# Optimization experiments

Measured on AMD Instinct MI355X. Metric: run time of the kernel, lower is better.

Reference implementation:

```python
import jax, jax.numpy as jnp
import numpy as np


def setup_inputs() -> dict:
    key = jax.random.key(0)
    k1, k2 = jax.random.split(key)
    b, n, d = 8, 8192, 512
    x = jax.random.normal(k1, (b, n, d), dtype=jnp.float32)
    # t holds 2n-2 Toeplitz coefficients per channel; forward only uses the first n rows.
    t = jax.random.normal(k2, (2 * n - 2, d), dtype=jnp.float32)
    return {"x": x, "t": t}


def reference(x, t):
    """Per-channel causal cumulative weighted sum (the math of the naive quadruple loop):
        o[i, u, j] = sum_{v=0}^{u} t[v, j] * x[i, v, j]
    x: (b, n, d), t: (2n-2, d) -> o: (b, n, d)
    """
    n = x.shape[1]
    # broadcast t over batch, fuse elementwise product, then inclusive cumsum along seq
    return jnp.cumsum(x * t[None, :n, :], axis=1)
```

## Files before the change

### kernel.cpp

```cpp
#include <hip/hip_runtime.h>


typedef float f4 __attribute__((ext_vector_type(4)));

#define D  512
#define DV (D / 4)
#define C  128
#define RS 4

__global__ __launch_bounds__(DV * RS) void k_chunksum(
    const float* __restrict__ x, const float* __restrict__ t,
    float* __restrict__ S, int b, int n, int L) {
  const int c  = blockIdx.x / b;
  const int i  = blockIdx.x % b;
  const int jv = threadIdx.x & (DV - 1);
  const int h  = threadIdx.x >> 7;
  const int rows = L / RS;
  const size_t row0 = (size_t)c * L + (size_t)h * rows;
  const f4* xp = (const f4*)x + ((size_t)i * n + row0) * DV + jv;
  const f4* tp = (const f4*)t + row0 * DV + jv;
  f4 acc = {0.f, 0.f, 0.f, 0.f};
#pragma unroll 8
  for (int v = 0; v < rows; ++v) {
    acc += xp[(size_t)v * DV] * tp[(size_t)v * DV];
  }
  __shared__ f4 red[RS][DV];
  red[h][jv] = acc;
  __syncthreads();
  if (h == 0) {
    f4 s = red[0][jv] + red[1][jv] + red[2][jv] + red[3][jv];
    ((f4*)S)[((size_t)c * b + i) * DV + jv] = s;
  }
}

__global__ __launch_bounds__(DV) void k_out(
    const float* __restrict__ x, const float* __restrict__ t,
    const float* __restrict__ S, float* __restrict__ o, int b, int n, int L) {
  const int c  = blockIdx.x / b;
  const int i  = blockIdx.x % b;
  const int jv = threadIdx.x;

  f4 acc = {0.f, 0.f, 0.f, 0.f};
  const f4* Sp = (const f4*)S + (size_t)i * DV + jv;
  const size_t cstride = (size_t)b * DV;
#pragma unroll 8
  for (int cp = 0; cp < c; ++cp) {
    acc += Sp[(size_t)cp * cstride];
  }

  const size_t row0  = (size_t)c * L;
  const size_t xbase = ((size_t)i * n + row0) * DV + jv;
  const f4* xp = (const f4*)x + xbase;
  const f4* tp = (const f4*)t + row0 * DV + jv;
  f4*       op = (f4*)o + xbase;
#pragma unroll 4
  for (int v = 0; v < L; ++v) {
    acc += xp[(size_t)v * DV] * tp[(size_t)v * DV];
    op[(size_t)v * DV] = acc;
  }
}

__global__ __launch_bounds__(256) void k_naive(
    const float* __restrict__ x, const float* __restrict__ t,
    float* __restrict__ o, int b, int n) {
  const int tid = blockIdx.x * 256 + threadIdx.x;
  if (tid >= b * DV) return;
  const int i  = tid / DV;
  const int jv = tid % DV;
  const f4* xp = (const f4*)x + (size_t)i * n * DV + jv;
  const f4* tp = (const f4*)t + jv;
  f4*       op = (f4*)o + (size_t)i * n * DV + jv;
  f4 acc = {0.f, 0.f, 0.f, 0.f};
  for (int v = 0; v < n; ++v) {
    acc += xp[(size_t)v * DV] * tp[(size_t)v * DV];
    op[(size_t)v * DV] = acc;
  }
}

extern "C" void kernel_launch(void* const* d_in, const int* in_sizes, int n_in,
                              void* d_out, int out_size, void* d_ws, size_t ws_size,
                              hipStream_t stream) {
  const float* x = (const float*)d_in[0];
  const float* t = (const float*)d_in[1];
  float*       o = (float*)d_out;

  const long long t_elems = in_sizes[1];
  const int n = (int)((t_elems / D + 2) / 2);
  const int b = (int)((long long)in_sizes[0] / ((long long)n * D));

  const size_t need = (size_t)C * b * D * sizeof(float);

  if (n % C == 0 && (n / C) % RS == 0 && ws_size >= need) {
    const int L = n / C;
    float* S = (float*)d_ws;
    hipLaunchKernelGGL(k_chunksum, dim3(C * b), dim3(DV * RS), 0, stream,
                       x, t, S, b, n, L);
    hipLaunchKernelGGL(k_out, dim3(C * b), dim3(DV), 0, stream,
                       x, t, S, o, b, n, L);
  } else {
    const int threads = b * DV;
    hipLaunchKernelGGL(k_naive, dim3((threads + 255) / 256), dim3(256), 0, stream,
                       x, t, o, b, n);
  }
}
```

Measured before the change: 300.8 us.

## Fuse chunk-sum and output passes into single-pass decoupled look-back scan

Replaces the two-kernel scan (chunk sums, then a rescan that re-reads x and t) with one kernel using a decoupled look-back. Blocks take ordered IDs from an atomic ticket, keep their products in registers, publish partial and inclusive sums with flags, and walk back over predecessor flags to build the prefix. This removes the second read of x and t and the O(C) prefix loop per block. In exchange it adds a memset, spin-waiting on flags across blocks, register pressure from holding 16 f4 per thread, and nontemporal stores for the output.

```diff
diff --git a/kernel.cpp b/kernel.cpp
--- a/kernel.cpp
+++ b/kernel.cpp
@@ -3,10 +3,102 @@
 
 typedef float f4 __attribute__((ext_vector_type(4)));
 
-#define D  512
-#define DV (D / 4)
-#define C  128
-#define RS 4
+#define D   512
+#define DV  128
+#define C   128
+#define BT  512
+#define RS  4
+#define RPT 16
+
+__global__ __launch_bounds__(BT, 4) void k_lookback(
+    const float* __restrict__ x, const float* __restrict__ t,
+    float* __restrict__ o, int b, int n,
+    unsigned* __restrict__ flags, unsigned* __restrict__ ticket,
+    float* __restrict__ Spart, float* __restrict__ Sincl) {
+
+  __shared__ unsigned s_vid;
+  __shared__ f4 red[RS][DV];
+  __shared__ f4 csum[DV];
+  __shared__ f4 pfx[DV];
+
+  if (threadIdx.x == 0) s_vid = atomicAdd(ticket, 1u);
+  __syncthreads();
+  const unsigned vid = s_vid;
+  const int c = (int)(vid / (unsigned)b);
+  const int i = (int)(vid % (unsigned)b);
+
+  const int jv = threadIdx.x & (DV - 1);
+  const int h  = threadIdx.x >> 7;
+  const int L  = n / C;
+  const size_t row0 = (size_t)c * L + (size_t)h * RPT;
+  const f4* xp = (const f4*)x + ((size_t)i * n + row0) * DV + jv;
+  const f4* tp = (const f4*)t + row0 * DV + jv;
+
+  f4 p[RPT];
+  f4 s = {0.f, 0.f, 0.f, 0.f};
+#pragma unroll
+  for (int v = 0; v < RPT; ++v) {
+    p[v] = xp[(size_t)v * DV] * tp[(size_t)v * DV];
+    s += p[v];
+  }
+  red[h][jv] = s;
+  __syncthreads();
+
+  if (threadIdx.x < DV) {
+    f4 cs = red[0][jv] + red[1][jv] + red[2][jv] + red[3][jv];
+    csum[jv] = cs;
+    if (c > 0) ((f4*)Spart)[(size_t)vid * DV + jv] = cs;
+  }
+  __syncthreads();
+  if (c > 0 && threadIdx.x == 0) {
+    __threadfence();
+    __hip_atomic_store(&flags[vid], 1u, __ATOMIC_RELEASE, __HIP_MEMORY_SCOPE_AGENT);
+  }
+
+  if (threadIdx.x < 64) {
+    const int l = threadIdx.x;
+    f4 pf0 = {0.f, 0.f, 0.f, 0.f}, pf1 = {0.f, 0.f, 0.f, 0.f};
+    int cp = c - 1;
+    while (cp >= 0) {
+      const unsigned pidx = (unsigned)cp * (unsigned)b + (unsigned)i;
+      unsigned st;
+      do {
+        st = __hip_atomic_load(&flags[pidx], __ATOMIC_ACQUIRE,
+                               __HIP_MEMORY_SCOPE_AGENT);
+      } while (st == 0u);
+      const f4* Sp = (st == 2u ? (const f4*)Sincl : (const f4*)Spart)
+                     + (size_t)pidx * DV;
+      pf0 += Sp[l];
+      pf1 += Sp[l + 64];
+      if (st == 2u) break;
+      --cp;
+    }
+    pfx[l]      = pf0;
+    pfx[l + 64] = pf1;
+    if (c + 1 < C) {
+      f4* Si = (f4*)Sincl + (size_t)vid * DV;
+      Si[l]      = pf0 + csum[l];
+      Si[l + 64] = pf1 + csum[l + 64];
+      __threadfence();
+      if (l == 0)
+        __hip_atomic_store(&flags[vid], 2u, __ATOMIC_RELEASE,
+                           __HIP_MEMORY_SCOPE_AGENT);
+    }
+  }
+  __syncthreads();
+
+  f4 acc = pfx[jv];
+#pragma unroll
+  for (int hh = 0; hh < RS - 1; ++hh)
+    if (hh < h) acc += red[hh][jv];
+
+  f4* op = (f4*)o + ((size_t)i * n + row0) * DV + jv;
+#pragma unroll
+  for (int v = 0; v < RPT; ++v) {
+    acc += p[v];
+    __builtin_nontemporal_store(acc, &op[(size_t)v * DV]);
+  }
+}
 
 __global__ __launch_bounds__(DV * RS) void k_chunksum(
     const float* __restrict__ x, const float* __restrict__ t,
@@ -20,10 +112,7 @@
   const f4* xp = (const f4*)x + ((size_t)i * n + row0) * DV + jv;
   const f4* tp = (const f4*)t + row0 * DV + jv;
   f4 acc = {0.f, 0.f, 0.f, 0.f};
-#pragma unroll 8
-  for (int v = 0; v < rows; ++v) {
-    acc += xp[(size_t)v * DV] * tp[(size_t)v * DV];
-  }
+  for (int v = 0; v < rows; ++v) acc += xp[(size_t)v * DV] * tp[(size_t)v * DV];
   __shared__ f4 red[RS][DV];
   red[h][jv] = acc;
   __syncthreads();
@@ -39,21 +128,15 @@
   const int c  = blockIdx.x / b;
   const int i  = blockIdx.x % b;
   const int jv = threadIdx.x;
-
   f4 acc = {0.f, 0.f, 0.f, 0.f};
   const f4* Sp = (const f4*)S + (size_t)i * DV + jv;
   const size_t cstride = (size_t)b * DV;
-#pragma unroll 8
-  for (int cp = 0; cp < c; ++cp) {
-    acc += Sp[(size_t)cp * cstride];
-  }
-
+  for (int cp = 0; cp < c; ++cp) acc += Sp[(size_t)cp * cstride];
   const size_t row0  = (size_t)c * L;
   const size_t xbase = ((size_t)i * n + row0) * DV + jv;
   const f4* xp = (const f4*)x + xbase;
   const f4* tp = (const f4*)t + row0 * DV + jv;
   f4*       op = (f4*)o + xbase;
-#pragma unroll 4
   for (int v = 0; v < L; ++v) {
     acc += xp[(size_t)v * DV] * tp[(size_t)v * DV];
     op[(size_t)v * DV] = acc;
@@ -88,14 +171,26 @@
   const int n = (int)((t_elems / D + 2) / 2);
   const int b = (int)((long long)in_sizes[0] / ((long long)n * D));
 
-  const size_t need = (size_t)C * b * D * sizeof(float);
-
-  if (n % C == 0 && (n / C) % RS == 0 && ws_size >= need) {
+  const int nb = C * b;
+  const size_t ctrl_bytes = 65536;
+  const size_t s_bytes    = (size_t)nb * D * sizeof(float);
+  const size_t need       = ctrl_bytes + 2 * s_bytes;
+
+  if (n % C == 0 && (n / C) == RS * RPT && ws_size >= need) {
+    unsigned* flags  = (unsigned*)d_ws;
+    unsigned* ticket = (unsigned*)d_ws + nb;
+    float* Spart = (float*)((char*)d_ws + ctrl_bytes);
+    float* Sincl = Spart + (size_t)nb * D;
+    hipMemsetAsync(d_ws, 0, ctrl_bytes, stream);
+    hipLaunchKernelGGL(k_lookback, dim3(nb), dim3(BT), 0, stream,
+                       x, t, o, b, n, flags, ticket, Spart, Sincl);
+  } else if (n % C == 0 && (n / C) % RS == 0 &&
+             ws_size >= (size_t)nb * D * sizeof(float)) {
     const int L = n / C;
     float* S = (float*)d_ws;
-    hipLaunchKernelGGL(k_chunksum, dim3(C * b), dim3(DV * RS), 0, stream,
+    hipLaunchKernelGGL(k_chunksum, dim3(nb), dim3(DV * RS), 0, stream,
                        x, t, S, b, n, L);
-    hipLaunchKernelGGL(k_out, dim3(C * b), dim3(DV), 0, stream,
+    hipLaunchKernelGGL(k_out, dim3(nb), dim3(DV), 0, stream,
                        x, t, S, o, b, n, L);
   } else {
     const int threads = b * DV;
```

New measurement: 502.6 us. 67.1% more time.
